# Optimization experiments

Hardware: AMD Instinct MI355X
Metric: run time of the kernel (lower is better)

## Reference

```python
import jax, jax.numpy as jnp
import numpy as np
from jax.scipy.special import logsumexp

B, T, LD, HD, K = 64, 2048, 16, 64, 8
TEMP = 1.0  # annealing=False
LOG2PI = float(np.log(2.0 * np.pi))


def setup_inputs() -> dict:
    key = jax.random.key(0)
    ks = jax.random.split(key, 10)
    return {
        "z": jax.random.normal(ks[0], (B, T, LD), jnp.float32),
        "pi": jax.random.normal(ks[1], (K,), jnp.float32) * 0.5,
        "Q": jax.random.normal(ks[2], (K, K), jnp.float32) * 0.5,
        "init_mean": jax.random.normal(ks[3], (K, LD), jnp.float32),
        # torch init: rand(K,1,1) * eye(LD) * 5  (a scale factor per state)
        "init_cov": jax.random.uniform(ks[4], (K, 1, 1), jnp.float32) * 5.0 * jnp.eye(LD, dtype=jnp.float32)[None],
        "covs": jnp.tile(jnp.eye(LD, dtype=jnp.float32)[None], (K, 1, 1)) + 0.05 * jax.random.normal(ks[5], (K, LD, LD), jnp.float32),
        "W1": jax.random.normal(ks[6], (K, HD, LD), jnp.float32) / np.sqrt(LD),
        "b1": jnp.zeros((K, HD), jnp.float32),
        "W2": jax.random.normal(ks[7], (K, LD, HD), jnp.float32) / np.sqrt(HD),
        "b2": jnp.zeros((K, LD), jnp.float32),
    }


def _chol_terms(C):
    """Sigma = C C^T + 1e-6 I ; return (L^{-1}, 0.5*logdet) per state."""
    dim = C.shape[-1]
    Sigma = C @ jnp.swapaxes(C, -1, -2) + 1e-6 * jnp.eye(dim, dtype=C.dtype)
    L = jnp.linalg.cholesky(Sigma)  # [K,D,D]
    Linv = jax.vmap(lambda l: jax.scipy.linalg.solve_triangular(l, jnp.eye(dim, dtype=C.dtype), lower=True))(L)
    logdet_half = jnp.sum(jnp.log(jnp.diagonal(L, axis1=-2, axis2=-1)), -1)  # [K]
    return Linv, logdet_half


def _mvn_logp(diff, Linv, logdet_half):
    # diff [B,t,K,D], Linv [K,D,D] -> [B,t,K]
    y = jnp.einsum('kde,btke->btkd', Linv, diff)
    maha = jnp.sum(y * y, -1)
    d = diff.shape[-1]
    return -0.5 * maha - logdet_half - 0.5 * d * LOG2PI


def reference(z, pi, Q, init_mean, init_cov, covs, W1, b1, W2, b2):
    # ---- local evidence: log p(z_1|s_1), log p(z_t | z_{t-1}, s_t)  [B,T,K]
    Linv0, ld0 = _chol_terms(init_cov)
    le1 = _mvn_logp(z[:, :1, None, :] - init_mean, Linv0, ld0)  # [B,1,K]
    zp = z[:, :-1]  # [B,T-1,D]
    h = jax.nn.softplus(jnp.einsum('btd,khd->btkh', zp, W1) + b1)  # per-state MLP hidden
    mu = jnp.einsum('btkh,kdh->btkd', h, W2) + b2  # [B,T-1,K,D]
    LinvT, ldT = _chol_terms(covs)
    leT = _mvn_logp(z[:, 1:, None, :] - mu, LinvT, ldT)  # [B,T-1,K]
    le = jnp.concatenate([le1, leT], axis=1)  # [B,T,K]

    # ---- alpha recursion (filtering)
    logpi = jax.nn.log_softmax(pi / TEMP)
    Qlog = jax.nn.log_softmax(Q / TEMP, axis=-1)  # log p(s_t=j | s_{t-1}=i)
    QT = Qlog.T  # [to, from]
    lp0 = le[:, 0] + logpi
    lz0 = logsumexp(lp0, -1)
    la0 = lp0 - lz0[:, None]
    le_rest = jnp.swapaxes(le[:, 1:], 0, 1)  # [T-1,B,K]

    def astep(la_prev, le_t):
        lp = logsumexp(le_t[:, :, None] + QT[None] + la_prev[:, None, :], axis=-1)
        lz = logsumexp(lp, -1)
        la = lp - lz[:, None]
        return la, (la, lz)

    _, (las, lzs) = jax.lax.scan(astep, la0, le_rest)
    log_alpha = jnp.concatenate([la0[:, None], jnp.swapaxes(las, 0, 1)], axis=1)  # [B,T,K]
    log_Z = jnp.concatenate([lz0[:, None], lzs.T], axis=1)  # [B,T]

    # ---- beta recursion (smoothing), reverse scan
    def bstep(lb_next, inp):
        le_t, lz_t = inp
        lb = logsumexp(Qlog[None] + le_t[:, None, :] + lb_next[:, None, :], axis=-1) - lz_t[:, None]
        return lb, lb

    _, lbs = jax.lax.scan(bstep, jnp.zeros((B, K), le.dtype), (le_rest, log_Z[:, 1:].T), reverse=True)
    log_beta = jnp.concatenate([jnp.swapaxes(lbs, 0, 1), jnp.zeros((B, 1, K), le.dtype)], axis=1)

    # ---- posteriors
    gamma = jnp.exp(log_alpha + log_beta)  # [B,T,K]
    paired = jnp.exp(Qlog[None, None] + log_alpha[:, :-1, :, None] + log_beta[:, 1:, None, :] + le[:, 1:, None, :] - log_Z[:, 1:, None, None])  # [B,T-1,K,K]
    return gamma, paired, log_Z
```

## Files before the change

### kernel.cpp

```cpp
#include <hip/hip_runtime.h>

#define B_ 64
#define T_ 2048
#define LD_ 16
#define HD_ 64
#define K_ 8
#define L_ 16
#define C_ 128
#define S_ 16

constexpr int OFF_LE    = 0;
constexpr int OFF_ALPHA = 1048576;
constexpr int OFF_EBAR  = 2097152;
constexpr int OFF_ZT    = OFF_ALPHA;
constexpr int OFF_PBUF  = 3145728;
constexpr int OFF_RLOG  = 3670016;
constexpr int OFF_AIN   = 3678208;
constexpr int OFF_SB    = 3743744;
constexpr int OFF_SBUF  = 3809280;
constexpr int OFF_UBUF  = 3874816;
constexpr int OFF_ULOG  = 3940352;
constexpr int OFF_SAIN  = 3941376;
constexpr int OFF_BENT  = 3949568;
constexpr int OFF_PRM   = 3957760;

constexpr int P_LINV0 = 0;
constexpr int P_LINVT = 2048;
constexpr int P_LD0   = 4096;
constexpr int P_LDT   = 4104;
constexpr int P_LOGPI = 4112;
constexpr int P_QEXP  = 4120;
constexpr int P_QTEXP = 4184;

constexpr int FI_NC2 = 32768;
constexpr int FI_C0I = 32896;

constexpr int OUT_PAIRED = B_*T_*K_;
constexpr int OUT_LOGZ   = OUT_PAIRED + B_*(T_-1)*K_*K_;

template<int CTRL>
__device__ __forceinline__ float dppmov(float x) {
  int xi = __float_as_int(x);
  int r = __builtin_amdgcn_update_dpp(xi, xi, CTRL, 0xF, 0xF, true);
  return __int_as_float(r);
}
__device__ __forceinline__ void allg8(float v, float w[8]) {
  w[0] = v;
  w[1] = dppmov<0xB1>(v);
  w[2] = dppmov<0x4E>(v);
  w[3] = dppmov<0x4E>(w[1]);
  w[7] = dppmov<0x141>(v);
  w[6] = dppmov<0xB1>(w[7]);
  w[5] = dppmov<0x4E>(w[7]);
  w[4] = dppmov<0x4E>(w[6]);
}
template<int V> __device__ __forceinline__ float xorg8(float x);
template<> __device__ __forceinline__ float xorg8<0>(float x) { return x; }
template<> __device__ __forceinline__ float xorg8<1>(float x) { return dppmov<0xB1>(x); }
template<> __device__ __forceinline__ float xorg8<2>(float x) { return dppmov<0x4E>(x); }
template<> __device__ __forceinline__ float xorg8<3>(float x) { return dppmov<0x4E>(dppmov<0xB1>(x)); }
template<> __device__ __forceinline__ float xorg8<4>(float x) { return dppmov<0x4E>(dppmov<0xB1>(dppmov<0x141>(x))); }
template<> __device__ __forceinline__ float xorg8<5>(float x) { return dppmov<0x4E>(dppmov<0x141>(x)); }
template<> __device__ __forceinline__ float xorg8<6>(float x) { return dppmov<0xB1>(dppmov<0x141>(x)); }
template<> __device__ __forceinline__ float xorg8<7>(float x) { return dppmov<0x141>(x); }

__device__ __forceinline__ float bfly_sum8(float x) {
  x += dppmov<0xB1>(x); x += dppmov<0x4E>(x); x += dppmov<0x141>(x); return x;
}
__device__ __forceinline__ float bfly_max8(float x) {
  x = fmaxf(x, dppmov<0xB1>(x)); x = fmaxf(x, dppmov<0x4E>(x)); x = fmaxf(x, dppmov<0x141>(x)); return x;
}
__device__ __forceinline__ float rcpnr(float x) {
  float r0 = __builtin_amdgcn_rcpf(x);
  return r0 * __builtin_fmaf(-x, r0, 2.0f);
}
__device__ __forceinline__ void col2row(const float cl[8], float rv[8]) {
  rv[0] = cl[0];
  rv[1] = xorg8<1>(cl[1]);
  rv[2] = xorg8<2>(cl[2]);
  rv[3] = xorg8<3>(cl[3]);
  rv[4] = xorg8<4>(cl[4]);
  rv[5] = xorg8<5>(cl[5]);
  rv[6] = xorg8<6>(cl[6]);
  rv[7] = xorg8<7>(cl[7]);
}
__device__ __forceinline__ void mmul8(const float a[8], const float m[8], float o[8]) {
  float m8[8][8];
  #pragma unroll
  for (int w = 0; w < 8; w++) allg8(m[w], m8[w]);
  #pragma unroll
  for (int v = 0; v < 8; v++) {
    float acc = 0.f;
    #pragma unroll
    for (int u = 0; u < 8; u++) acc = __builtin_fmaf(a[u], m8[u^v][u], acc);
    o[v] = acc;
  }
}
__device__ __forceinline__ float maxnorm8(float m[8]) {
  float mx = m[0];
  #pragma unroll
  for (int u = 1; u < 8; u++) mx = fmaxf(mx, m[u]);
  mx = bfly_max8(mx);
  float r = rcpnr(mx);
  #pragma unroll
  for (int u = 0; u < 8; u++) m[u] *= r;
  return mx;
}
__device__ __forceinline__ void load_rows(const float* p, float r[8]) {
  const float4* q = (const float4*)p;
  float4 x0 = q[0], x1 = q[1];
  r[0]=x0.x; r[1]=x0.y; r[2]=x0.z; r[3]=x0.w;
  r[4]=x1.x; r[5]=x1.y; r[6]=x1.z; r[7]=x1.w;
}

typedef __attribute__((ext_vector_type(4))) float f32x4;
typedef __attribute__((ext_vector_type(8))) short bf16x8;

__device__ __forceinline__ unsigned ph(float a, float b) {
  return (__float_as_uint(a) >> 16) | (__float_as_uint(b) & 0xFFFF0000u);
}
__device__ __forceinline__ float hif(float a) {
  return __uint_as_float(__float_as_uint(a) & 0xFFFF0000u);
}
__device__ __forceinline__ bf16x8 u2f(uint4 u) {
  return __builtin_bit_cast(bf16x8, u);
}
__device__ __forceinline__ bf16x8 mkfrag(float4 v) {
  unsigned ux = __float_as_uint(v.x), uy = __float_as_uint(v.y);
  unsigned uz = __float_as_uint(v.z), uw = __float_as_uint(v.w);
  unsigned h01 = (ux >> 16) | (uy & 0xFFFF0000u);
  unsigned h23 = (uz >> 16) | (uw & 0xFFFF0000u);
  float lx = v.x - __uint_as_float(ux & 0xFFFF0000u);
  float ly = v.y - __uint_as_float(uy & 0xFFFF0000u);
  float lz = v.z - __uint_as_float(uz & 0xFFFF0000u);
  float lw = v.w - __uint_as_float(uw & 0xFFFF0000u);
  unsigned l01 = ph(lx, ly);
  unsigned l23 = ph(lz, lw);
  return u2f(make_uint4(h01, h23, l01, l23));
}
__device__ __forceinline__ f32x4 MF(bf16x8 a, bf16x8 b, f32x4 c) {
  return __builtin_amdgcn_mfma_f32_16x16x32_bf16(a, b, c, 0, 0, 0);
}

__global__ __launch_bounds__(64) void prep_kernel(
    const float* __restrict__ pi, const float* __restrict__ Q,
    const float* __restrict__ init_cov, const float* __restrict__ covs,
    float* __restrict__ prm)
{
  int tid = threadIdx.x;
  int blk = blockIdx.x;
  if (blk < 16) {
    int k = blk & 7;
    const float* C = (blk < 8 ? init_cov : covs) + k*256;
    float* outL  = prm + (blk < 8 ? P_LINV0 : P_LINVT) + k*256;
    float* outld = prm + (blk < 8 ? P_LD0   : P_LDT)   + k;
    __shared__ float S[16][17], L[16][17], X[16][17];
    for (int e = tid; e < 256; e += 64) {
      int r = e >> 4, c = e & 15;
      float s = (r == c) ? 1e-6f : 0.f;
      for (int l = 0; l < 16; l++) s += C[r*16+l] * C[c*16+l];
      S[r][c] = s;
    }
    __syncthreads();
    for (int j = 0; j < 16; j++) {
      if (tid == 0) L[j][j] = sqrtf(S[j][j]);
// ... 81 lines not shown
    F4[6144 + ((k*2+kc)*4+q)*16 + d] =
        make_uint4(ph(v[0],v[1]), ph(v[2],v[3]), ph(v[4],v[5]), ph(v[6],v[7]));
    F4[7168 + ((k*2+kc)*4+q)*16 + d] =
        make_uint4(ph(lo[0],lo[1]), ph(lo[2],lo[3]), ph(lo[4],lo[5]), ph(lo[6],lo[7]));
  }
  for (int mt = 0; mt < 4; mt++) {
    int hh = 16*mt + d;
    float v[4], lo[4];
    for (int j = 0; j < 4; j++) { v[j] = W1[k*1024 + hh*16 + 4*q + j]; lo[j] = v[j] - hif(v[j]); }
    unsigned x = ph(v[0],v[1]), y = ph(v[2],v[3]);
    F4[((k*4+mt)*4+q)*16 + d]        = make_uint4(x, y, x, y);
    F4[2048 + ((k*4+mt)*4+q)*16 + d] = make_uint4(ph(lo[0],lo[1]), ph(lo[2],lo[3]), 0u, 0u);
  }
  {
    float v[4], lo[4];
    for (int j = 0; j < 4; j++) { v[j] = Ls[d][4*q+j]; lo[j] = v[j] - hif(v[j]); }
    unsigned x = ph(v[0],v[1]), y = ph(v[2],v[3]);
    F4[4096 + (k*4+q)*16 + d] = make_uint4(x, y, x, y);
    F4[4608 + (k*4+q)*16 + d] = make_uint4(ph(lo[0],lo[1]), ph(lo[2],lo[3]), 0u, 0u);
    for (int j = 0; j < 4; j++) { v[j] = L0s[d][4*q+j]; lo[j] = v[j] - hif(v[j]); }
    x = ph(v[0],v[1]); y = ph(v[2],v[3]);
    F4[5120 + (k*4+q)*16 + d] = make_uint4(x, y, x, y);
    F4[5632 + (k*4+q)*16 + d] = make_uint4(ph(lo[0],lo[1]), ph(lo[2],lo[3]), 0u, 0u);
  }
  if (q == 0) {
    float s2 = 0.f, s0 = 0.f;
    for (int e = 0; e < 16; e++) {
      s2 += Ls[d][e]  * b2[k*16+e];
      s0 += L0s[d][e] * init_mean[k*16+e];
    }
    frag[FI_NC2 + k*16 + d] = -s2;
    frag[FI_C0I + k*16 + d] = -s0;
  }
}

__global__ __launch_bounds__(256) void ztr_kernel(
    const float* __restrict__ z, float* __restrict__ zt)
{
  int tid = blockIdx.x*256 + threadIdx.x;
  int t = tid >> 6, b = tid & 63;
  const float4* src = (const float4*)(z + (b*T_ + t)*LD_);
  float4* dst = (float4*)(zt + t*1024 + b*16);
  dst[0] = src[0]; dst[1] = src[1]; dst[2] = src[2]; dst[3] = src[3];
}

__global__ __launch_bounds__(256) void emisB_kernel(
    const float* __restrict__ zt, const float* __restrict__ b1,
    const float* __restrict__ frag, const float* __restrict__ prm,
    float* __restrict__ lebuf)
{
  int lane = threadIdx.x & 63;
  int wid = __builtin_amdgcn_readfirstlane(blockIdx.x*4 + (threadIdx.x >> 6));
  int bblk = wid & 3;
  int tch  = (wid >> 2) & 127;
  int k    = wid >> 9;
  int c = lane & 15, q = lane >> 4;
  int b = bblk*16 + c;
  const uint4* F4 = (const uint4*)frag;

  bf16x8 w1a1[4], w1a2[4];
  #pragma unroll
  for (int mt = 0; mt < 4; mt++) {
    w1a1[mt] = u2f(F4[((k*4+mt)*4+q)*16 + c]);
    w1a2[mt] = u2f(F4[2048 + ((k*4+mt)*4+q)*16 + c]);
  }
  bf16x8 lva1 = u2f(F4[4096 + (k*4+q)*16 + c]);
  bf16x8 lva2 = u2f(F4[4608 + (k*4+q)*16 + c]);
  bf16x8 gahi[2], galo[2];
  #pragma unroll
  for (int kc = 0; kc < 2; kc++) {
    gahi[kc] = u2f(F4[6144 + ((k*2+kc)*4+q)*16 + c]);
    galo[kc] = u2f(F4[7168 + ((k*2+kc)*4+q)*16 + c]);
  }
  float b1iv[16];
  #pragma unroll
  for (int i = 0; i < 16; i++)
    b1iv[i] = b1[k*64 + (i>>2)*16 + 4*q + (i&3)];
  float nc2[4];
  #pragma unroll
  for (int r = 0; r < 4; r++) nc2[r] = frag[FI_NC2 + k*16 + 4*q + r];
  float lconst = -prm[P_LDT + k] - 14.70301653f;

  int t0 = tch*16;
  bf16x8 zp;
  int ttstart;
  if (tch == 0) {
    float4 zv0 = *(const float4*)(zt + b*16 + 4*q);
    bf16x8 zc0 = mkfrag(zv0);
    bf16x8 l0a1 = u2f(F4[5120 + (k*4+q)*16 + c]);
    bf16x8 l0a2 = u2f(F4[5632 + (k*4+q)*16 + c]);
    f32x4 acc;
    acc[0] = frag[FI_C0I + k*16 + 4*q + 0];
    acc[1] = frag[FI_C0I + k*16 + 4*q + 1];
    acc[2] = frag[FI_C0I + k*16 + 4*q + 2];
    acc[3] = frag[FI_C0I + k*16 + 4*q + 3];
    acc = MF(l0a1, zc0, acc);
    acc = MF(l0a2, zc0, acc);
    float m2 = (acc[0]*acc[0] + acc[1]*acc[1]) + (acc[2]*acc[2] + acc[3]*acc[3]);
    m2 += __shfl_xor(m2, 16);
    m2 += __shfl_xor(m2, 32);
    float le = -0.5f*m2 - prm[P_LD0+k] - 14.70301653f + prm[P_LOGPI+k];
    if (q == 0) lebuf[k*64 + b] = le;
    zp = zc0;
    ttstart = 1;
  } else {
    float4 zvp = *(const float4*)(zt + (t0-1)*1024 + b*16 + 4*q);
    zp = mkfrag(zvp);
    ttstart = 0;
  }

  float4 zv = *(const float4*)(zt + (t0+ttstart)*1024 + b*16 + 4*q);
  #pragma unroll 1
  for (int tt = ttstart; tt < 16; tt++) {
    int t = t0 + tt;
    float4 zvn;
    if (tt < 15) zvn = *(const float4*)(zt + (t+1)*1024 + b*16 + 4*q);
    bf16x8 zc = mkfrag(zv);
    f32x4 a1[4];
    #pragma unroll
    for (int mt = 0; mt < 4; mt++) {
      f32x4 ai;
      ai[0] = b1iv[mt*4+0]; ai[1] = b1iv[mt*4+1];
      ai[2] = b1iv[mt*4+2]; ai[3] = b1iv[mt*4+3];
      ai = MF(w1a1[mt], zp, ai);
      a1[mt] = MF(w1a2[mt], zp, ai);
    }
    float hv[16];
    #pragma unroll
    for (int i = 0; i < 16; i++) {
      float a = a1[i>>2][i&3];
      hv[i] = fmaxf(a, 0.f) + __logf(1.f + __expf(-fabsf(a)));
    }
    bf16x8 hhi[2], hlo[2];
    #pragma unroll
    for (int kc = 0; kc < 2; kc++) {
      const float* hp = hv + 8*kc;
      hhi[kc] = u2f(make_uint4(ph(hp[0],hp[1]), ph(hp[2],hp[3]),
                               ph(hp[4],hp[5]), ph(hp[6],hp[7])));
      float l0 = hp[0]-hif(hp[0]), l1 = hp[1]-hif(hp[1]);
      float l2 = hp[2]-hif(hp[2]), l3 = hp[3]-hif(hp[3]);
      float l4 = hp[4]-hif(hp[4]), l5 = hp[5]-hif(hp[5]);
      float l6 = hp[6]-hif(hp[6]), l7 = hp[7]-hif(hp[7]);
      hlo[kc] = u2f(make_uint4(ph(l0,l1), ph(l2,l3), ph(l4,l5), ph(l6,l7)));
    }
    f32x4 acc;
    acc[0] = nc2[0]; acc[1] = nc2[1]; acc[2] = nc2[2]; acc[3] = nc2[3];
    acc = MF(lva1, zc, acc);
    acc = MF(lva2, zc, acc);
    #pragma unroll
    for (int kc = 0; kc < 2; kc++) {
      acc = MF(gahi[kc], hhi[kc], acc);
      acc = MF(galo[kc], hhi[kc], acc);
      acc = MF(gahi[kc], hlo[kc], acc);
    }
    float m2 = (acc[0]*acc[0] + acc[1]*acc[1]) + (acc[2]*acc[2] + acc[3]*acc[3]);
    m2 += __shfl_xor(m2, 16);
    m2 += __shfl_xor(m2, 32);
    float le = -0.5f*m2 + lconst;
    if (q == 0) lebuf[t*512 + k*64 + b] = le;
    zp = zc;
    zv = zvn;
  }
}

__global__ __launch_bounds__(256) void fwdP1_kernel(
    const float* __restrict__ lebuf, const float* __restrict__ prm,
    float* __restrict__ pbuf)
{
  int g = (blockIdx.x*256 + threadIdx.x) >> 3;
  int j = threadIdx.x & 7;
  int b = g & 63, c = g >> 6;
  float qtv[64];
  #pragma unroll
  for (int u = 0; u < 8; u++)
    #pragma unroll
    for (int v = 0; v < 8; v++)
      qtv[u*8+v] = prm[P_QTEXP + (j^u)*8 + (j^v)];
  float lev[16];
  #pragma unroll
  for (int u = 0; u < 16; u++) lev[u] = lebuf[(c*L_+u)*512 + j*64 + b];
  float pl[8];
  int ustart;
  if (c == 0) {
    float m = bfly_max8(lev[0]);
    float e = __expf(lev[0]-m);
    allg8(e, pl);
    ustart = 1;
  } else {
    #pragma unroll
    for (int u = 0; u < 8; u++) pl[u] = (u == 0) ? 1.f : 0.f;
    ustart = 0;
  }
  for (int s = ustart; s < 16; s++) {
    float m = bfly_max8(lev[s]);
    float e = __expf(lev[s]-m);
    float e8[8]; allg8(e, e8);
    float np[8];
    #pragma unroll
    for (int u = 0; u < 8; u++) {
      float acc = 0.f;
      #pragma unroll
      for (int v = 0; v < 8; v++) acc = __builtin_fmaf(qtv[u*8+v], pl[v], acc);
      np[u] = e8[u] * acc;
    }
    float mx = np[0];
    #pragma unroll
    for (int u = 1; u < 8; u++) mx = fmaxf(mx, np[u]);
    mx = bfly_max8(mx);
    float r = rcpnr(mx);
    #pragma unroll
    for (int u = 0; u < 8; u++) pl[u] = np[u] * r;
  }
  float rv[8]; col2row(pl, rv);
  float4* dst = (float4*)(pbuf + g*64 + j*8);
  dst[0] = make_float4(rv[0], rv[1], rv[2], rv[3]);
  dst[1] = make_float4(rv[4], rv[5], rv[6], rv[7]);
}

__global__ __launch_bounds__(256) void fwdP2a_kernel(
    const float* __restrict__ pbuf, float* __restrict__ sbuf)
{
  int g = (blockIdx.x*256 + threadIdx.x) >> 3;
  int i = threadIdx.x & 7;
  int b = g & 63, s = g >> 6;
  float m[8];
  load_rows(pbuf + ((8*s)*64 + b)*64 + i*8, m);
  for (int c = 8*s+1; c <= 8*s+7; c++) {
    float a[8];
    load_rows(pbuf + (c*64 + b)*64 + i*8, a);
    float nm[8];
    mmul8(a, m, nm);
    maxnorm8(nm);
    #pragma unroll
    for (int v = 0; v < 8; v++) m[v] = nm[v];
  }
  float4* dst = (float4*)(sbuf + (s*64 + b)*64 + i*8);
  dst[0] = make_float4(m[0], m[1], m[2], m[3]);
  dst[1] = make_float4(m[4], m[5], m[6], m[7]);
}

__global__ __launch_bounds__(512) void fwdP2b_kernel(
    const float* __restrict__ sbuf, float* __restrict__ sain)
{
  int lane = threadIdx.x;
  int b = lane >> 3, i = lane & 7;
  const float4* base = (const float4*)sbuf;
  float4 c0 = base[(0*64+b)*16 + i*2], c1 = base[(0*64+b)*16 + i*2 + 1];
  float a = 0.125f;
  for (int s = 0; s < 16; s++) {
    int s2 = (s < 15) ? s+1 : 15;
    float4 n0 = base[(s2*64+b)*16 + i*2], n1 = base[(s2*64+b)*16 + i*2 + 1];
    float aw[8]; allg8(a, aw);
    float sm = ((c0.x*aw[0] + c0.y*aw[1]) + (c0.z*aw[2] + c0.w*aw[3]))
             + ((c1.x*aw[4] + c1.y*aw[5]) + (c1.z*aw[6] + c1.w*aw[7]));
    float tot = bfly_sum8(sm);
    float an = sm * rcpnr(tot);
    if (s < 15) { a = an; sain[(s+1)*512 + b*8 + i] = a; }
    c0 = n0; c1 = n1;
  }
}

__global__ __launch_bounds__(256) void fwdP2c_kernel(
    const float* __restrict__ pbuf, const float* __restrict__ sain,
    float* __restrict__ ain)
{
  int g = (blockIdx.x*256 + threadIdx.x) >> 3;
  int i = threadIdx.x & 7;
  int b = g & 63, s = g >> 6;
  float a = (s == 0) ? 0.125f : sain[s*512 + b*8 + i];
  ain[(8*s)*512 + b*8 + i] = a;
  for (int u = 0; u < 7; u++) {
    int c = 8*s + u;
    float r[8];
    load_rows(pbuf + (c*64 + b)*64 + i*8, r);
    float aw[8]; allg8(a, aw);
    float sm = ((r[0]*aw[0] + r[1]*aw[1]) + (r[2]*aw[2] + r[3]*aw[3]))
             + ((r[4]*aw[4] + r[5]*aw[5]) + (r[6]*aw[6] + r[7]*aw[7]));
    float tot = bfly_sum8(sm);
    a = sm * rcpnr(tot);
    ain[(c+1)*512 + b*8 + i] = a;
  }
}

__global__ __launch_bounds__(256) void fwdP3_kernel(
    const float* __restrict__ lebuf, const float* __restrict__ prm,
    const float* __restrict__ ain, float* __restrict__ alpha,
    float* __restrict__ ebar, float* __restrict__ rbuf,
    float* __restrict__ rlog, float* __restrict__ out)
{
  int g = (blockIdx.x*256 + threadIdx.x) >> 3;
  int i = threadIdx.x & 7;
  int b = g & 63, c = g >> 6;
  int off = b*8 + i;
  float q[8];
  #pragma unroll
  for (int u = 0; u < 8; u++) q[u] = prm[P_QTEXP + i*8 + (i^u)];
  float lev[16];
  #pragma unroll
  for (int u = 0; u < 16; u++) lev[u] = lebuf[(c*L_+u)*512 + i*64 + b];
  float* logZ = out + OUT_LOGZ + b*T_;
  float eb_loc[16];
  float a;
  int ustart;
  if (c == 0) {
    float m0 = bfly_max8(lev[0]);
    float e0 = __expf(lev[0]-m0);
    float ct = bfly_sum8(e0);
    float r = rcpnr(ct);
    a = e0 * r;
    alpha[off] = a;
    eb_loc[0] = a;
    ebar[off] = a;
    if (i == 0) logZ[0] = m0 + __logf(ct);
    ustart = 1;
  } else {
    a = ain[c*512 + off];
    ustart = 0;
  }
  for (int u = ustart; u < 16; u++) {
    int t = c*L_ + u;
    float m = bfly_max8(lev[u]);
    float e = __expf(lev[u]-m);
    float w[8]; allg8(a, w);
    float dot = ((q[0]*w[0]+q[1]*w[1]) + (q[2]*w[2]+q[3]*w[3]))
              + ((q[4]*w[4]+q[5]*w[5]) + (q[6]*w[6]+q[7]*w[7]));
    float p = e * dot;
    float ct = bfly_sum8(p);
    float r = rcpnr(ct);
    a = p * r;
    alpha[t*512 + off] = a;
    float eb = e * r;
    eb_loc[u] = eb;
    ebar[t*512 + off] = eb;
    if (i == 0) logZ[t] = m + __logf(ct);
  }
  float qv[64];
  #pragma unroll
  for (int u = 0; u < 8; u++)
    #pragma unroll
    for (int v = 0; v < 8; v++)
      qv[u*8+v] = prm[P_QEXP + (i^u)*8 + (i^v)];
  float rl[8];
  #pragma unroll
  for (int u = 0; u < 8; u++) rl[u] = (u == 0) ? 1.f : 0.f;
  float lsc = 0.f;
  #pragma unroll
  for (int s = 15; s >= 1; s--) {
    float e8[8]; allg8(eb_loc[s], e8);
    float nr[8];
    #pragma unroll
    for (int u = 0; u < 8; u++) {
      float acc = 0.f;
      #pragma unroll
      for (int v = 0; v < 8; v++) acc = __builtin_fmaf(qv[u*8+v], e8[v]*rl[v], acc);
      nr[u] = acc;
    }
    float mx = nr[0];
    #pragma unroll
    for (int u = 1; u < 8; u++) mx = fmaxf(mx, nr[u]);
    mx = bfly_max8(mx);
    float r = rcpnr(mx);
    #pragma unroll
    for (int u = 0; u < 8; u++) rl[u] = nr[u] * r;
    lsc += __logf(mx);
  }
  float rv[8]; col2row(rl, rv);
  float4* dst = (float4*)(rbuf + g*64 + i*8);
  dst[0] = make_float4(rv[0], rv[1], rv[2], rv[3]);
  dst[1] = make_float4(rv[4], rv[5], rv[6], rv[7]);
  if (i == 0) rlog[g] = lsc;
}

__global__ __launch_bounds__(256) void bwdP2a_kernel(
    const float* __restrict__ rbuf, const float* __restrict__ rlog,
    const float* __restrict__ ebar, const float* __restrict__ prm,
    float* __restrict__ ubuf, float* __restrict__ ulog)
{
  int g = (blockIdx.x*256 + threadIdx.x) >> 3;
  int i = threadIdx.x & 7;
  int b = g & 63, s = g >> 6;
  float qr[8];
  #pragma unroll
  for (int u = 0; u < 8; u++) qr[u] = prm[P_QEXP + i*8 + (i^u)];
  float m[8], lsum;
  {
    int c = 8*s + 7;
    float r[8];
    load_rows(rbuf + (c*64 + b)*64 + i*8, r);
    float e = ebar[(c*L_)*512 + b*8 + i];
    float d[8];
    #pragma unroll
    for (int v = 0; v < 8; v++) d[v] = e * r[v];
    mmul8(qr, d, m);
    lsum = rlog[c*64 + b] + __logf(maxnorm8(m));
  }
  for (int c = 8*s + 6; c >= 8*s; c--) {
    float r[8];
    load_rows(rbuf + (c*64 + b)*64 + i*8, r);
    float e = ebar[(c*L_)*512 + b*8 + i];
    float t[8];
    mmul8(r, m, t);
    #pragma unroll
    for (int v = 0; v < 8; v++) t[v] *= e;
    float nm[8];
    mmul8(qr, t, nm);
    lsum += rlog[c*64 + b] + __logf(maxnorm8(nm));
    #pragma unroll
    for (int v = 0; v < 8; v++) m[v] = nm[v];
  }
  float4* dst = (float4*)(ubuf + (s*64 + b)*64 + i*8);
  dst[0] = make_float4(m[0], m[1], m[2], m[3]);
  dst[1] = make_float4(m[4], m[5], m[6], m[7]);
  if (i == 0) ulog[s*64 + b] = lsum;
}

__global__ __launch_bounds__(512) void bwdP2b_kernel(
    const float* __restrict__ ubuf, const float* __restrict__ ulog,
    float* __restrict__ bent)
{
  int lane = threadIdx.x;
  int b = lane >> 3, i = lane & 7;
  bent[15*512 + b*8 + i] = 1.f;
  const float4* base = (const float4*)ubuf;
  float sh = 1.f, sig = 0.f;
  float4 c0 = base[(15*64+b)*16 + i*2], c1 = base[(15*64+b)*16 + i*2 + 1];
  float cu = ulog[15*64 + b];
  for (int s = 15; s >= 1; s--) {
    int s2 = (s > 1) ? s-1 : 1;
    float4 n0 = base[(s2*64+b)*16 + i*2], n1 = base[(s2*64+b)*16 + i*2 + 1];
    float nu = ulog[s2*64 + b];
    float sw[8]; allg8(sh, sw);
    float y = ((c0.x*sw[0] + c0.y*sw[1]) + (c0.z*sw[2] + c0.w*sw[3]))
            + ((c1.x*sw[4] + c1.y*sw[5]) + (c1.z*sw[6] + c1.w*sw[7]));
    float mx = bfly_max8(y);
    sh = y * rcpnr(mx);
    sig += cu + __logf(mx);
    bent[(s-1)*512 + b*8 + i] = sh * __expf(sig);
    c0 = n0; c1 = n1; cu = nu;
  }
}

__global__ __launch_bounds__(256) void bwdP2c_kernel(
    const float* __restrict__ rbuf, const float* __restrict__ rlog,
    const float* __restrict__ ebar, const float* __restrict__ prm,
    const float* __restrict__ bent, float* __restrict__ sb)
{
  int g = (blockIdx.x*256 + threadIdx.x) >> 3;
  int i = threadIdx.x & 7;
  int b = g & 63, s = g >> 6;
  float qr[8];
  #pragma unroll
  for (int u = 0; u < 8; u++) qr[u] = prm[P_QEXP + i*8 + (i^u)];
  float bt = bent[s*512 + b*8 + i];
  for (int c = 8*s + 7; c >= 8*s; c--) {
    float r[8];
    load_rows(rbuf + (c*64 + b)*64 + i*8, r);
    float e = ebar[(c*L_)*512 + b*8 + i];
    float rl = rlog[c*64 + b];
    float btw[8]; allg8(bt, btw);
    float y = ((r[0]*btw[0] + r[1]*btw[1]) + (r[2]*btw[2] + r[3]*btw[3]))
            + ((r[4]*btw[4] + r[5]*btw[5]) + (r[6]*btw[6] + r[7]*btw[7]));
    y *= __expf(rl);
    sb[c*512 + b*8 + i] = y;
    float w[8]; allg8(e*y, w);
    float nb = 0.f;
    #pragma unroll
    for (int v = 0; v < 8; v++) nb = __builtin_fmaf(qr[v], w[v], nb);
    bt = nb;
  }
}

__global__ __launch_bounds__(256) void bwdP3_kernel(
    const float* __restrict__ alpha, const float* __restrict__ ebar,
    const float* __restrict__ sb, const float* __restrict__ prm,
    float* __restrict__ out)
{
  int g = (blockIdx.x*256 + threadIdx.x) >> 3;
  int i = threadIdx.x & 7;
  int b = g & 63, c = g >> 6;
  int off = b*8 + i;
  float q[8];
  #pragma unroll
  for (int u = 0; u < 8; u++) q[u] = prm[P_QEXP + i*8 + (i^u)];
  float av[16], ev[16];
  #pragma unroll
  for (int u = 0; u < 16; u++) av[u] = alpha[(c*L_+u)*512 + off];
  #pragma unroll
  for (int u = 1; u < 16; u++) ev[u] = ebar[(c*L_+u)*512 + off];
  float* po = out + OUT_PAIRED + b*((T_-1)*64);
  float* go = out + b*(T_*K_);
  float bb;
  if (c == 127) {
    bb = 1.f;
    go[2047*8 + i] = av[15];
  } else {
    float ev16 = ebar[((c+1)*L_)*512 + off];
    float sbv  = sb[(c+1)*512 + off];
    float w[8]; allg8(ev16*sbv, w);
    bb = ((q[0]*w[0]+q[1]*w[1]) + (q[2]*w[2]+q[3]*w[3]))
       + ((q[4]*w[4]+q[5]*w[5]) + (q[6]*w[6]+q[7]*w[7]));
    int t = c*L_ + 15;
    #pragma unroll
    for (int u2 = 0; u2 < 8; u2++)
      po[t*64 + i*8 + (i^u2)] = av[15] * q[u2] * w[u2];
    go[t*8 + i] = av[15] * bb;
  }
  #pragma unroll
  for (int u = 15; u >= 1; u--) {
    float w[8]; allg8(ev[u]*bb, w);
    float nb = ((q[0]*w[0]+q[1]*w[1]) + (q[2]*w[2]+q[3]*w[3]))
             + ((q[4]*w[4]+q[5]*w[5]) + (q[6]*w[6]+q[7]*w[7]));
    int t = c*L_ + u - 1;
    #pragma unroll
    for (int u2 = 0; u2 < 8; u2++)
      po[t*64 + i*8 + (i^u2)] = av[u-1] * q[u2] * w[u2];
    go[t*8 + i] = av[u-1] * nb;
    bb = nb;
  }
}

extern "C" void kernel_launch(void* const* d_in, const int* in_sizes, int n_in,
                              void* d_out, int out_size, void* d_ws, size_t ws_size,
                              hipStream_t stream) {
  const float* z         = (const float*)d_in[0];
  const float* pi        = (const float*)d_in[1];
  const float* Q         = (const float*)d_in[2];
  const float* init_mean = (const float*)d_in[3];
  const float* init_cov  = (const float*)d_in[4];
  const float* covs      = (const float*)d_in[5];
  const float* W1        = (const float*)d_in[6];
  const float* b1        = (const float*)d_in[7];
  const float* W2        = (const float*)d_in[8];
  const float* b2        = (const float*)d_in[9];
  float* out = (float*)d_out;
  float* ws  = (float*)d_ws;

  prep_kernel<<<17, 64, 0, stream>>>(pi, Q, init_cov, covs, ws + OFF_PRM);
  prep2_kernel<<<8, 64, 0, stream>>>(W1, W2, b2, init_mean, ws + OFF_PRM,
                                     ws + OFF_UBUF);
  ztr_kernel<<<512, 256, 0, stream>>>(z, ws + OFF_ZT);
  emisB_kernel<<<1024, 256, 0, stream>>>(ws + OFF_ZT, b1, ws + OFF_UBUF,
                                         ws + OFF_PRM, ws + OFF_LE);
  fwdP1_kernel<<<256, 256, 0, stream>>>(ws + OFF_LE, ws + OFF_PRM, ws + OFF_PBUF);
  fwdP2a_kernel<<<32, 256, 0, stream>>>(ws + OFF_PBUF, ws + OFF_SBUF);
  fwdP2b_kernel<<<1, 512, 0, stream>>>(ws + OFF_SBUF, ws + OFF_SAIN);
  fwdP2c_kernel<<<32, 256, 0, stream>>>(ws + OFF_PBUF, ws + OFF_SAIN, ws + OFF_AIN);
  fwdP3_kernel<<<256, 256, 0, stream>>>(ws + OFF_LE, ws + OFF_PRM, ws + OFF_AIN,
                                        ws + OFF_ALPHA, ws + OFF_EBAR,
                                        ws + OFF_PBUF, ws + OFF_RLOG, out);
  bwdP2a_kernel<<<32, 256, 0, stream>>>(ws + OFF_PBUF, ws + OFF_RLOG,
                                        ws + OFF_EBAR, ws + OFF_PRM,
                                        ws + OFF_UBUF, ws + OFF_ULOG);
  bwdP2b_kernel<<<1, 512, 0, stream>>>(ws + OFF_UBUF, ws + OFF_ULOG, ws + OFF_BENT);
  bwdP2c_kernel<<<32, 256, 0, stream>>>(ws + OFF_PBUF, ws + OFF_RLOG,
                                        ws + OFF_EBAR, ws + OFF_PRM,
                                        ws + OFF_BENT, ws + OFF_SB);
  bwdP3_kernel<<<256, 256, 0, stream>>>(ws + OFF_ALPHA, ws + OFF_EBAR,
                                        ws + OFF_SB, ws + OFF_PRM, out);
}
```

Measured before the change: 245.4 us.

## Fuse HMM scan phases into fewer kernels via in-block shared-memory chunk combines

Result: faster. 230.8 us (-5.9%).

```diff
diff --git a/kernel.cpp b/kernel.cpp
--- a/kernel.cpp
+++ b/kernel.cpp
@@ -15,8 +15,6 @@
 constexpr int OFF_ZT    = OFF_ALPHA;
 constexpr int OFF_PBUF  = 3145728;
 constexpr int OFF_RLOG  = 3670016;
-constexpr int OFF_AIN   = 3678208;
-constexpr int OFF_SB    = 3743744;
 constexpr int OFF_SBUF  = 3809280;
 constexpr int OFF_UBUF  = 3874816;
 constexpr int OFF_ULOG  = 3940352;
@@ -74,6 +72,17 @@
   float r0 = __builtin_amdgcn_rcpf(x);
   return r0 * __builtin_fmaf(-x, r0, 2.0f);
 }
+__device__ __forceinline__ void absg8(float v, float w[8]) {
+  int x = __float_as_int(v);
+  w[0] = __int_as_float(__builtin_amdgcn_ds_swizzle(x, 0x18));
+  w[1] = __int_as_float(__builtin_amdgcn_ds_swizzle(x, 0x38));
+  w[2] = __int_as_float(__builtin_amdgcn_ds_swizzle(x, 0x58));
+  w[3] = __int_as_float(__builtin_amdgcn_ds_swizzle(x, 0x78));
+  w[4] = __int_as_float(__builtin_amdgcn_ds_swizzle(x, 0x98));
+  w[5] = __int_as_float(__builtin_amdgcn_ds_swizzle(x, 0xB8));
+  w[6] = __int_as_float(__builtin_amdgcn_ds_swizzle(x, 0xD8));
+  w[7] = __int_as_float(__builtin_amdgcn_ds_swizzle(x, 0xF8));
+}
 __device__ __forceinline__ void col2row(const float cl[8], float rv[8]) {
   rv[0] = cl[0];
   rv[1] = xorg8<1>(cl[1]);
@@ -111,6 +120,10 @@
   float4 x0 = q[0], x1 = q[1];
   r[0]=x0.x; r[1]=x0.y; r[2]=x0.z; r[3]=x0.w;
   r[4]=x1.x; r[5]=x1.y; r[6]=x1.z; r[7]=x1.w;
+}
+__device__ __forceinline__ float dotw8(const float r[8], const float w[8]) {
+  return ((r[0]*w[0]+r[1]*w[1]) + (r[2]*w[2]+r[3]*w[3]))
+       + ((r[4]*w[4]+r[5]*w[5]) + (r[6]*w[6]+r[7]*w[7]));
 }
 
 typedef __attribute__((ext_vector_type(4))) float f32x4;
@@ -298,8 +311,8 @@
   int lane = threadIdx.x & 63;
   int wid = __builtin_amdgcn_readfirstlane(blockIdx.x*4 + (threadIdx.x >> 6));
   int bblk = wid & 3;
-  int tch  = (wid >> 2) & 127;
-  int k    = wid >> 9;
+  int tch  = (wid >> 2) & 255;
+  int k    = wid >> 10;
   int c = lane & 15, q = lane >> 4;
   int b = bblk*16 + c;
   const uint4* F4 = (const uint4*)frag;
@@ -327,7 +340,7 @@
   for (int r = 0; r < 4; r++) nc2[r] = frag[FI_NC2 + k*16 + 4*q + r];
   float lconst = -prm[P_LDT + k] - 14.70301653f;
 
-  int t0 = tch*16;
+  int t0 = tch*8;
   bf16x8 zp;
   int ttstart;
   if (tch == 0) {
@@ -357,10 +370,10 @@
 
   float4 zv = *(const float4*)(zt + (t0+ttstart)*1024 + b*16 + 4*q);
   #pragma unroll 1
-  for (int tt = ttstart; tt < 16; tt++) {
+  for (int tt = ttstart; tt < 8; tt++) {
     int t = t0 + tt;
-    float4 zvn;
-    if (tt < 15) zvn = *(const float4*)(zt + (t+1)*1024 + b*16 + 4*q);
+    float4 zvn = zv;
+    if (tt < 7) zvn = *(const float4*)(zt + (t+1)*1024 + b*16 + 4*q);
     bf16x8 zc = mkfrag(zv);
     f32x4 a1[4];
     #pragma unroll
@@ -409,80 +422,92 @@
   }
 }
 
-__global__ __launch_bounds__(256) void fwdP1_kernel(
+__global__ __launch_bounds__(256) void fwdA_kernel(
     const float* __restrict__ lebuf, const float* __restrict__ prm,
-    float* __restrict__ pbuf)
+    float* __restrict__ pbuf, float* __restrict__ sbuf)
 {
-  int g = (blockIdx.x*256 + threadIdx.x) >> 3;
-  int j = threadIdx.x & 7;
-  int b = g & 63, c = g >> 6;
+  int lane64 = threadIdx.x & 63;
+  int iu = threadIdx.x >> 6;
+  int unit = blockIdx.x*4 + iu;
+  int b = unit & 63, s = unit >> 6;
+  int u = lane64 >> 3, j = lane64 & 7;
+  int c = 8*s + u;
   float qtv[64];
   #pragma unroll
-  for (int u = 0; u < 8; u++)
+  for (int x = 0; x < 8; x++)
     #pragma unroll
     for (int v = 0; v < 8; v++)
-      qtv[u*8+v] = prm[P_QTEXP + (j^u)*8 + (j^v)];
+      qtv[x*8+v] = prm[P_QTEXP + (j^x)*8 + (j^v)];
   float lev[16];
   #pragma unroll
-  for (int u = 0; u < 16; u++) lev[u] = lebuf[(c*L_+u)*512 + j*64 + b];
+  for (int x = 0; x < 16; x++) lev[x] = lebuf[(c*L_+x)*512 + j*64 + b];
   float pl[8];
-  int ustart;
   if (c == 0) {
     float m = bfly_max8(lev[0]);
     float e = __expf(lev[0]-m);
     allg8(e, pl);
-    ustart = 1;
   } else {
-    #pragma unroll
-    for (int u = 0; u < 8; u++) pl[u] = (u == 0) ? 1.f : 0.f;
-    ustart = 0;
-  }
-  for (int s = ustart; s < 16; s++) {
-    float m = bfly_max8(lev[s]);
-    float e = __expf(lev[s]-m);
+    float m = bfly_max8(lev[0]);
+    float e = __expf(lev[0]-m);
     float e8[8]; allg8(e, e8);
     float np[8];
     #pragma unroll
-    for (int u = 0; u < 8; u++) {
+    for (int x = 0; x < 8; x++) np[x] = e8[x] * qtv[x*8];
+    float mx = np[0];
+    #pragma unroll
+    for (int x = 1; x < 8; x++) mx = fmaxf(mx, np[x]);
+    mx = bfly_max8(mx);
+    float r = rcpnr(mx);
+    #pragma unroll
+    for (int x = 0; x < 8; x++) pl[x] = np[x] * r;
+  }
+  #pragma unroll
+  for (int sx = 1; sx < 16; sx++) {
+    float m = bfly_max8(lev[sx]);
+    float e = __expf(lev[sx]-m);
+    float e8[8]; allg8(e, e8);
+    float np[8];
+    #pragma unroll
+    for (int x = 0; x < 8; x++) {
       float acc = 0.f;
       #pragma unroll
-      for (int v = 0; v < 8; v++) acc = __builtin_fmaf(qtv[u*8+v], pl[v], acc);
-      np[u] = e8[u] * acc;
+      for (int v = 0; v < 8; v++) acc = __builtin_fmaf(qtv[x*8+v], pl[v], acc);
+      np[x] = e8[x] * acc;
     }
     float mx = np[0];
     #pragma unroll
-    for (int u = 1; u < 8; u++) mx = fmaxf(mx, np[u]);
+    for (int x = 1; x < 8; x++) mx = fmaxf(mx, np[x]);
     mx = bfly_max8(mx);
     float r = rcpnr(mx);
     #pragma unroll
-    for (int u = 0; u < 8; u++) pl[u] = np[u] * r;
+    for (int x = 0; x < 8; x++) pl[x] = np[x] * r;
   }
   float rv[8]; col2row(pl, rv);
-  float4* dst = (float4*)(pbuf + g*64 + j*8);
+  float4* dst = (float4*)(pbuf + (c*64 + b)*64 + j*8);
   dst[0] = make_float4(rv[0], rv[1], rv[2], rv[3]);
   dst[1] = make_float4(rv[4], rv[5], rv[6], rv[7]);
-}
-
-__global__ __launch_bounds__(256) void fwdP2a_kernel(
-    const float* __restrict__ pbuf, float* __restrict__ sbuf)
-{
-  int g = (blockIdx.x*256 + threadIdx.x) >> 3;
-  int i = threadIdx.x & 7;
-  int b = g & 63, s = g >> 6;
-  float m[8];
-  load_rows(pbuf + ((8*s)*64 + b)*64 + i*8, m);
-  for (int c = 8*s+1; c <= 8*s+7; c++) {
-    float a[8];
-    load_rows(pbuf + (c*64 + b)*64 + i*8, a);
-    float nm[8];
-    mmul8(a, m, nm);
-    maxnorm8(nm);
-    #pragma unroll
-    for (int v = 0; v < 8; v++) m[v] = nm[v];
-  }
-  float4* dst = (float4*)(sbuf + (s*64 + b)*64 + i*8);
-  dst[0] = make_float4(m[0], m[1], m[2], m[3]);
-  dst[1] = make_float4(m[4], m[5], m[6], m[7]);
+  __shared__ float M[4][8][64];
+  #pragma unroll
+  for (int v = 0; v < 8; v++) M[iu][u][j*8+v] = rv[v];
+  __syncthreads();
+  if (u == 0) {
+    float m[8];
+    #pragma unroll
+    for (int v = 0; v < 8; v++) m[v] = M[iu][0][j*8+v];
+    for (int cc = 1; cc < 8; cc++) {
+      float a[8];
+      #pragma unroll
+      for (int v = 0; v < 8; v++) a[v] = M[iu][cc][j*8+v];
+      float nm[8];
+      mmul8(a, m, nm);
+      maxnorm8(nm);
+      #pragma unroll
+      for (int v = 0; v < 8; v++) m[v] = nm[v];
+    }
+    float4* d2 = (float4*)(sbuf + (s*64 + b)*64 + j*8);
+    d2[0] = make_float4(m[0], m[1], m[2], m[3]);
+    d2[1] = make_float4(m[4], m[5], m[6], m[7]);
+  }
 }
 
 __global__ __launch_bounds__(512) void fwdP2b_kernel(
@@ -506,158 +531,159 @@
   }
 }
 
-__global__ __launch_bounds__(256) void fwdP2c_kernel(
-    const float* __restrict__ pbuf, const float* __restrict__ sain,
-    float* __restrict__ ain)
+__global__ __launch_bounds__(256) void fwdB_kernel(
+    const float* __restrict__ lebuf, const float* __restrict__ prm,
+    const float* __restrict__ sain, float* pbuf,
+    float* __restrict__ alpha, float* __restrict__ ebar,
+    float* __restrict__ rlog, float* __restrict__ ubuf,
+    float* __restrict__ ulog, float* __restrict__ out)
 {
-  int g = (blockIdx.x*256 + threadIdx.x) >> 3;
-  int i = threadIdx.x & 7;
-  int b = g & 63, s = g >> 6;
-  float a = (s == 0) ? 0.125f : sain[s*512 + b*8 + i];
-  ain[(8*s)*512 + b*8 + i] = a;
-  for (int u = 0; u < 7; u++) {
-    int c = 8*s + u;
-    float r[8];
-    load_rows(pbuf + (c*64 + b)*64 + i*8, r);
-    float aw[8]; allg8(a, aw);
-    float sm = ((r[0]*aw[0] + r[1]*aw[1]) + (r[2]*aw[2] + r[3]*aw[3]))
-             + ((r[4]*aw[4] + r[5]*aw[5]) + (r[6]*aw[6] + r[7]*aw[7]));
-    float tot = bfly_sum8(sm);
-    a = sm * rcpnr(tot);
-    ain[(c+1)*512 + b*8 + i] = a;
-  }
-}
-
-__global__ __launch_bounds__(256) void fwdP3_kernel(
-    const float* __restrict__ lebuf, const float* __restrict__ prm,
-    const float* __restrict__ ain, float* __restrict__ alpha,
-    float* __restrict__ ebar, float* __restrict__ rbuf,
-    float* __restrict__ rlog, float* __restrict__ out)
-{
-  int g = (blockIdx.x*256 + threadIdx.x) >> 3;
-  int i = threadIdx.x & 7;
-  int b = g & 63, c = g >> 6;
+  int lane64 = threadIdx.x & 63;
+  int iu = threadIdx.x >> 6;
+  int unit = blockIdx.x*4 + iu;
+  int b = unit & 63, s = unit >> 6;
+  int u = lane64 >> 3, i = lane64 & 7;
+  int c = 8*s + u;
   int off = b*8 + i;
+  __shared__ float Als[4][8];
+  __shared__ float Mh[4][8][64];
+  __shared__ float Lh[4][8];
+  float pr[8];
+  load_rows(pbuf + (c*64 + b)*64 + i*8, pr);
+  float lev[16];
+  #pragma unroll
+  for (int x = 0; x < 16; x++) lev[x] = lebuf[(c*L_+x)*512 + i*64 + b];
+  float av_in = 0.f;
+  if (u == 0) av_in = (s == 0) ? 0.125f : sain[s*512 + off];
+  for (int r = 0; r < 7; r++) {
+    if (u == r) {
+      if (r > 0) av_in = Als[iu][i];
+      float aw[8]; allg8(av_in, aw);
+      float sm = dotw8(pr, aw);
+      float tot = bfly_sum8(sm);
+      Als[iu][i] = sm * rcpnr(tot);
+    }
+    __syncthreads();
+  }
+  if (u == 7) av_in = Als[iu][i];
   float q[8];
   #pragma unroll
-  for (int u = 0; u < 8; u++) q[u] = prm[P_QTEXP + i*8 + (i^u)];
-  float lev[16];
-  #pragma unroll
-  for (int u = 0; u < 16; u++) lev[u] = lebuf[(c*L_+u)*512 + i*64 + b];
+  for (int x = 0; x < 8; x++) q[x] = prm[P_QTEXP + i*8 + (i^x)];
   float* logZ = out + OUT_LOGZ + b*T_;
   float eb_loc[16];
   float a;
-  int ustart;
   if (c == 0) {
     float m0 = bfly_max8(lev[0]);
-    float e0 = __expf(lev[0]-m0);
-    float ct = bfly_sum8(e0);
-    float r = rcpnr(ct);
-    a = e0 * r;
+    float e0x = __expf(lev[0]-m0);
+    float ct = bfly_sum8(e0x);
+    float rr = rcpnr(ct);
+    a = e0x * rr;
     alpha[off] = a;
     eb_loc[0] = a;
     ebar[off] = a;
     if (i == 0) logZ[0] = m0 + __logf(ct);
-    ustart = 1;
   } else {
-    a = ain[c*512 + off];
-    ustart = 0;
-  }
-  for (int u = ustart; u < 16; u++) {
-    int t = c*L_ + u;
-    float m = bfly_max8(lev[u]);
-    float e = __expf(lev[u]-m);
+    a = av_in;
+    int t = c*L_;
+    float m = bfly_max8(lev[0]);
+    float e = __expf(lev[0]-m);
     float w[8]; allg8(a, w);
-    float dot = ((q[0]*w[0]+q[1]*w[1]) + (q[2]*w[2]+q[3]*w[3]))
-              + ((q[4]*w[4]+q[5]*w[5]) + (q[6]*w[6]+q[7]*w[7]));
+    float dot = dotw8(q, w);
     float p = e * dot;
     float ct = bfly_sum8(p);
-    float r = rcpnr(ct);
-    a = p * r;
+    float rr = rcpnr(ct);
+    a = p * rr;
     alpha[t*512 + off] = a;
-    float eb = e * r;
-    eb_loc[u] = eb;
+    float eb = e * rr;
+    eb_loc[0] = eb;
     ebar[t*512 + off] = eb;
     if (i == 0) logZ[t] = m + __logf(ct);
   }
+  #pragma unroll
+  for (int x = 1; x < 16; x++) {
+    int t = c*L_ + x;
+    float m = bfly_max8(lev[x]);
+    float e = __expf(lev[x]-m);
+    float w[8]; allg8(a, w);
+    float dot = dotw8(q, w);
+    float p = e * dot;
+    float ct = bfly_sum8(p);
+    float rr = rcpnr(ct);
+    a = p * rr;
+    alpha[t*512 + off] = a;
+    float eb = e * rr;
+    eb_loc[x] = eb;
+    ebar[t*512 + off] = eb;
+    if (i == 0) logZ[t] = m + __logf(ct);
+  }
   float qv[64];
   #pragma unroll
-  for (int u = 0; u < 8; u++)
+  for (int x = 0; x < 8; x++)
     #pragma unroll
     for (int v = 0; v < 8; v++)
-      qv[u*8+v] = prm[P_QEXP + (i^u)*8 + (i^v)];
-  float rl[8];
-  #pragma unroll
-  for (int u = 0; u < 8; u++) rl[u] = (u == 0) ? 1.f : 0.f;
+      qv[x*8+v] = prm[P_QEXP + (i^x)*8 + (i^v)];
+  float rl8[8];
+  #pragma unroll
+  for (int x = 0; x < 8; x++) rl8[x] = (x == 0) ? 1.f : 0.f;
   float lsc = 0.f;
   #pragma unroll
-  for (int s = 15; s >= 1; s--) {
-    float e8[8]; allg8(eb_loc[s], e8);
+  for (int sx = 15; sx >= 1; sx--) {
+    float e8[8]; allg8(eb_loc[sx], e8);
     float nr[8];
     #pragma unroll
-    for (int u = 0; u < 8; u++) {
+    for (int x = 0; x < 8; x++) {
       float acc = 0.f;
       #pragma unroll
-      for (int v = 0; v < 8; v++) acc = __builtin_fmaf(qv[u*8+v], e8[v]*rl[v], acc);
-      nr[u] = acc;
+      for (int v = 0; v < 8; v++) acc = __builtin_fmaf(qv[x*8+v], e8[v]*rl8[v], acc);
+      nr[x] = acc;
     }
     float mx = nr[0];
     #pragma unroll
-    for (int u = 1; u < 8; u++) mx = fmaxf(mx, nr[u]);
+    for (int x = 1; x < 8; x++) mx = fmaxf(mx, nr[x]);
     mx = bfly_max8(mx);
     float r = rcpnr(mx);
     #pragma unroll
-    for (int u = 0; u < 8; u++) rl[u] = nr[u] * r;
+    for (int x = 0; x < 8; x++) rl8[x] = nr[x] * r;
     lsc += __logf(mx);
   }
-  float rv[8]; col2row(rl, rv);
-  float4* dst = (float4*)(rbuf + g*64 + i*8);
-  dst[0] = make_float4(rv[0], rv[1], rv[2], rv[3]);
-  dst[1] = make_float4(rv[4], rv[5], rv[6], rv[7]);
-  if (i == 0) rlog[g] = lsc;
-}
-
-__global__ __launch_bounds__(256) void bwdP2a_kernel(
-    const float* __restrict__ rbuf, const float* __restrict__ rlog,
-    const float* __restrict__ ebar, const float* __restrict__ prm,
-    float* __restrict__ ubuf, float* __restrict__ ulog)
-{
-  int g = (blockIdx.x*256 + threadIdx.x) >> 3;
-  int i = threadIdx.x & 7;
-  int b = g & 63, s = g >> 6;
+  float rv[8]; col2row(rl8, rv);
+  float4* dstR = (float4*)(pbuf + (c*64 + b)*64 + i*8);
+  dstR[0] = make_float4(rv[0], rv[1], rv[2], rv[3]);
+  dstR[1] = make_float4(rv[4], rv[5], rv[6], rv[7]);
+  if (i == 0) rlog[c*64 + b] = lsc;
   float qr[8];
   #pragma unroll
-  for (int u = 0; u < 8; u++) qr[u] = prm[P_QEXP + i*8 + (i^u)];
-  float m[8], lsum;
-  {
-    int c = 8*s + 7;
-    float r[8];
-    load_rows(rbuf + (c*64 + b)*64 + i*8, r);
-    float e = ebar[(c*L_)*512 + b*8 + i];
-    float d[8];
-    #pragma unroll
-    for (int v = 0; v < 8; v++) d[v] = e * r[v];
-    mmul8(qr, d, m);
-    lsum = rlog[c*64 + b] + __logf(maxnorm8(m));
-  }
-  for (int c = 8*s + 6; c >= 8*s; c--) {
-    float r[8];
-    load_rows(rbuf + (c*64 + b)*64 + i*8, r);
-    float e = ebar[(c*L_)*512 + b*8 + i];
-    float t[8];
-    mmul8(r, m, t);
-    #pragma unroll
-    for (int v = 0; v < 8; v++) t[v] *= e;
-    float nm[8];
-    mmul8(qr, t, nm);
-    lsum += rlog[c*64 + b] + __logf(maxnorm8(nm));
-    #pragma unroll
-    for (int v = 0; v < 8; v++) m[v] = nm[v];
-  }
-  float4* dst = (float4*)(ubuf + (s*64 + b)*64 + i*8);
-  dst[0] = make_float4(m[0], m[1], m[2], m[3]);
-  dst[1] = make_float4(m[4], m[5], m[6], m[7]);
-  if (i == 0) ulog[s*64 + b] = lsum;
+  for (int x = 0; x < 8; x++) qr[x] = prm[P_QEXP + i*8 + (i^x)];
+  float d8[8];
+  #pragma unroll
+  for (int v = 0; v < 8; v++) d8[v] = eb_loc[0] * rv[v];
+  float h8[8];
+  mmul8(qr, d8, h8);
+  float ls = lsc + __logf(maxnorm8(h8));
+  #pragma unroll
+  for (int v = 0; v < 8; v++) Mh[iu][u][i*8+v] = h8[v];
+  if (i == 0) Lh[iu][u] = ls;
+  __syncthreads();
+  if (u == 0) {
+    float m[8];
+    #pragma unroll
+    for (int v = 0; v < 8; v++) m[v] = Mh[iu][7][i*8+v];
+    float lsum = Lh[iu][7];
+    for (int cc = 6; cc >= 0; cc--) {
+      float aa[8];
+      #pragma unroll
+      for (int v = 0; v < 8; v++) aa[v] = Mh[iu][cc][i*8+v];
+      float t8[8];
+      mmul8(aa, m, t8);
+      lsum += Lh[iu][cc] + __logf(maxnorm8(t8));
+      #pragma unroll
+      for (int v = 0; v < 8; v++) m[v] = t8[v];
+    }
+    float4* d2 = (float4*)(ubuf + (s*64 + b)*64 + i*8);
+    d2[0] = make_float4(m[0], m[1], m[2], m[3]);
+    d2[1] = make_float4(m[4], m[5], m[6], m[7]);
+    if (i == 0) ulog[s*64 + b] = lsum;
+  }
 }
 
 __global__ __launch_bounds__(512) void bwdP2b_kernel(
@@ -686,82 +712,79 @@
   }
 }
 
-__global__ __launch_bounds__(256) void bwdP2c_kernel(
+__global__ __launch_bounds__(256) void bwdC_kernel(
+    const float* __restrict__ alpha, const float* __restrict__ ebar,
     const float* __restrict__ rbuf, const float* __restrict__ rlog,
-    const float* __restrict__ ebar, const float* __restrict__ prm,
-    const float* __restrict__ bent, float* __restrict__ sb)
-{
-  int g = (blockIdx.x*256 + threadIdx.x) >> 3;
-  int i = threadIdx.x & 7;
-  int b = g & 63, s = g >> 6;
-  float qr[8];
-  #pragma unroll
-  for (int u = 0; u < 8; u++) qr[u] = prm[P_QEXP + i*8 + (i^u)];
-  float bt = bent[s*512 + b*8 + i];
-  for (int c = 8*s + 7; c >= 8*s; c--) {
-    float r[8];
-    load_rows(rbuf + (c*64 + b)*64 + i*8, r);
-    float e = ebar[(c*L_)*512 + b*8 + i];
-    float rl = rlog[c*64 + b];
-    float btw[8]; allg8(bt, btw);
-    float y = ((r[0]*btw[0] + r[1]*btw[1]) + (r[2]*btw[2] + r[3]*btw[3]))
-            + ((r[4]*btw[4] + r[5]*btw[5]) + (r[6]*btw[6] + r[7]*btw[7]));
-    y *= __expf(rl);
-    sb[c*512 + b*8 + i] = y;
-    float w[8]; allg8(e*y, w);
-    float nb = 0.f;
-    #pragma unroll
-    for (int v = 0; v < 8; v++) nb = __builtin_fmaf(qr[v], w[v], nb);
-    bt = nb;
-  }
-}
-
-__global__ __launch_bounds__(256) void bwdP3_kernel(
-    const float* __restrict__ alpha, const float* __restrict__ ebar,
-    const float* __restrict__ sb, const float* __restrict__ prm,
+    const float* __restrict__ prm, const float* __restrict__ bent,
     float* __restrict__ out)
 {
-  int g = (blockIdx.x*256 + threadIdx.x) >> 3;
-  int i = threadIdx.x & 7;
-  int b = g & 63, c = g >> 6;
+  int lane64 = threadIdx.x & 63;
+  int iu = threadIdx.x >> 6;
+  int unit = blockIdx.x*4 + iu;
+  int b = unit & 63, s = unit >> 6;
+  int u = lane64 >> 3, i = lane64 & 7;
+  int c = 8*s + u;
   int off = b*8 + i;
-  float q[8];
-  #pragma unroll
-  for (int u = 0; u < 8; u++) q[u] = prm[P_QEXP + i*8 + (i^u)];
+  float qr[8], qa[8];
+  #pragma unroll
+  for (int x = 0; x < 8; x++) qr[x] = prm[P_QEXP + i*8 + (i^x)];
+  #pragma unroll
+  for (int v = 0; v < 8; v++) qa[v] = prm[P_QEXP + i*8 + v];
+  float r8[8];
+  load_rows(rbuf + (c*64 + b)*64 + i*8, r8);
+  float e0 = ebar[(c*L_)*512 + off];
+  float erl = __expf(rlog[c*64 + b]);
   float av[16], ev[16];
   #pragma unroll
-  for (int u = 0; u < 16; u++) av[u] = alpha[(c*L_+u)*512 + off];
-  #pragma unroll
-  for (int u = 1; u < 16; u++) ev[u] = ebar[(c*L_+u)*512 + off];
+  for (int x = 0; x < 16; x++) av[x] = alpha[(c*L_+x)*512 + off];
+  #pragma unroll
+  for (int x = 1; x < 16; x++) ev[x] = ebar[(c*L_+x)*512 + off];
+  float avm1 = (c > 0) ? alpha[(c*L_-1)*512 + off] : 0.f;
+  __shared__ float Bls[4][8];
+  float bt = 0.f, y = 0.f, nbv = 0.f;
+  for (int r = 7; r >= 0; r--) {
+    if (u == r) {
+      bt = (r == 7) ? bent[s*512 + off] : Bls[iu][i];
+      float bw[8]; allg8(bt, bw);
+      y = dotw8(r8, bw) * erl;
+      float ey = e0 * y;
+      float w[8]; allg8(ey, w);
+      nbv = 0.f;
+      #pragma unroll
+      for (int v = 0; v < 8; v++) nbv = __builtin_fmaf(qr[v], w[v], nbv);
+      if (r > 0) Bls[iu][i] = nbv;
+    }
+    __syncthreads();
+  }
   float* po = out + OUT_PAIRED + b*((T_-1)*64);
   float* go = out + b*(T_*K_);
-  float bb;
-  if (c == 127) {
-    bb = 1.f;
-    go[2047*8 + i] = av[15];
-  } else {
-    float ev16 = ebar[((c+1)*L_)*512 + off];
-    float sbv  = sb[(c+1)*512 + off];
-    float w[8]; allg8(ev16*sbv, w);
-    bb = ((q[0]*w[0]+q[1]*w[1]) + (q[2]*w[2]+q[3]*w[3]))
-       + ((q[4]*w[4]+q[5]*w[5]) + (q[6]*w[6]+q[7]*w[7]));
-    int t = c*L_ + 15;
-    #pragma unroll
-    for (int u2 = 0; u2 < 8; u2++)
-      po[t*64 + i*8 + (i^u2)] = av[15] * q[u2] * w[u2];
-    go[t*8 + i] = av[15] * bb;
-  }
-  #pragma unroll
-  for (int u = 15; u >= 1; u--) {
-    float w[8]; allg8(ev[u]*bb, w);
-    float nb = ((q[0]*w[0]+q[1]*w[1]) + (q[2]*w[2]+q[3]*w[3]))
-             + ((q[4]*w[4]+q[5]*w[5]) + (q[6]*w[6]+q[7]*w[7]));
-    int t = c*L_ + u - 1;
-    #pragma unroll
-    for (int u2 = 0; u2 < 8; u2++)
-      po[t*64 + i*8 + (i^u2)] = av[u-1] * q[u2] * w[u2];
-    go[t*8 + i] = av[u-1] * nb;
+  float bb = bt;
+  if (c == 127) go[2047*8 + i] = av[15];
+  #pragma unroll
+  for (int x = 15; x >= 1; x--) {
+    float eya[8]; absg8(ev[x]*bb, eya);
+    float term[8];
+    #pragma unroll
+    for (int v = 0; v < 8; v++) term[v] = qa[v]*eya[v];
+    float nb = ((term[0]+term[1]) + (term[2]+term[3]))
+             + ((term[4]+term[5]) + (term[6]+term[7]));
+    int t = c*L_ + x - 1;
+    float am = av[x-1];
+    float4* pd = (float4*)(po + t*64 + i*8);
+    pd[0] = make_float4(am*term[0], am*term[1], am*term[2], am*term[3]);
+    pd[1] = make_float4(am*term[4], am*term[5], am*term[6], am*term[7]);
+    go[t*8 + i] = am*nb;
     bb = nb;
+  }
+  if (c > 0) {
+    float eya[8]; absg8(e0*y, eya);
+    int t = c*L_ - 1;
+    float4* pd = (float4*)(po + t*64 + i*8);
+    pd[0] = make_float4(avm1*qa[0]*eya[0], avm1*qa[1]*eya[1],
+                        avm1*qa[2]*eya[2], avm1*qa[3]*eya[3]);
+    pd[1] = make_float4(avm1*qa[4]*eya[4], avm1*qa[5]*eya[5],
+                        avm1*qa[6]*eya[6], avm1*qa[7]*eya[7]);
+    go[t*8 + i] = avm1 * nbv;
   }
 }
 
@@ -785,22 +808,17 @@
   prep2_kernel<<<8, 64, 0, stream>>>(W1, W2, b2, init_mean, ws + OFF_PRM,
                                      ws + OFF_UBUF);
   ztr_kernel<<<512, 256, 0, stream>>>(z, ws + OFF_ZT);
-  emisB_kernel<<<1024, 256, 0, stream>>>(ws + OFF_ZT, b1, ws + OFF_UBUF,
+  emisB_kernel<<<2048, 256, 0, stream>>>(ws + OFF_ZT, b1, ws + OFF_UBUF,
                                          ws + OFF_PRM, ws + OFF_LE);
-  fwdP1_kernel<<<256, 256, 0, stream>>>(ws + OFF_LE, ws + OFF_PRM, ws + OFF_PBUF);
-  fwdP2a_kernel<<<32, 256, 0, stream>>>(ws + OFF_PBUF, ws + OFF_SBUF);
+  fwdA_kernel<<<256, 256, 0, stream>>>(ws + OFF_LE, ws + OFF_PRM,
+                                       ws + OFF_PBUF, ws + OFF_SBUF);
   fwdP2b_kernel<<<1, 512, 0, stream>>>(ws + OFF_SBUF, ws + OFF_SAIN);
-  fwdP2c_kernel<<<32, 256, 0, stream>>>(ws + OFF_PBUF, ws + OFF_SAIN, ws + OFF_AIN);
-  fwdP3_kernel<<<256, 256, 0, stream>>>(ws + OFF_LE, ws + OFF_PRM, ws + OFF_AIN,
-                                        ws + OFF_ALPHA, ws + OFF_EBAR,
-                                        ws + OFF_PBUF, ws + OFF_RLOG, out);
-  bwdP2a_kernel<<<32, 256, 0, stream>>>(ws + OFF_PBUF, ws + OFF_RLOG,
-                                        ws + OFF_EBAR, ws + OFF_PRM,
-                                        ws + OFF_UBUF, ws + OFF_ULOG);
+  fwdB_kernel<<<256, 256, 0, stream>>>(ws + OFF_LE, ws + OFF_PRM, ws + OFF_SAIN,
+                                       ws + OFF_PBUF, ws + OFF_ALPHA,
+                                       ws + OFF_EBAR, ws + OFF_RLOG,
+                                       ws + OFF_UBUF, ws + OFF_ULOG, out);
   bwdP2b_kernel<<<1, 512, 0, stream>>>(ws + OFF_UBUF, ws + OFF_ULOG, ws + OFF_BENT);
-  bwdP2c_kernel<<<32, 256, 0, stream>>>(ws + OFF_PBUF, ws + OFF_RLOG,
-                                        ws + OFF_EBAR, ws + OFF_PRM,
-                                        ws + OFF_BENT, ws + OFF_SB);
-  bwdP3_kernel<<<256, 256, 0, stream>>>(ws + OFF_ALPHA, ws + OFF_EBAR,
-                                        ws + OFF_SB, ws + OFF_PRM, out);
-}
+  bwdC_kernel<<<256, 256, 0, stream>>>(ws + OFF_ALPHA, ws + OFF_EBAR,
+                                       ws + OFF_PBUF, ws + OFF_RLOG,
+                                       ws + OFF_PRM, ws + OFF_BENT, out);
+}
```
